# Performance work log

Hardware: AMD Instinct MI355X
Metric: run time of the kernel (lower is better)

Reference implementation:

```python
import jax, jax.numpy as jnp
import numpy as np

N_NODES = 100000
N_EDGES = 250000
EMB = 32
NUM_RELS2 = 100   # 2 * num_rels
NUM_TYPES = 16


def _xavier(key, shape):
    fan_in, fan_out = shape[-2], shape[-1]
    limit = float(np.sqrt(6.0 / (fan_in + fan_out)))
    return jax.random.uniform(key, shape, jnp.float32, -limit, limit)


def setup_inputs() -> dict:
    key = jax.random.key(0)
    ks = jax.random.split(key, 9)
    src_ids = jax.random.randint(ks[0], (N_NODES,), 0, N_NODES)
    edge_src = jax.random.randint(ks[1], (N_EDGES,), 0, N_NODES)
    edge_dst = jax.random.randint(ks[2], (N_EDGES,), 0, N_NODES)
    etype = jax.random.randint(ks[3], (N_EDGES,), 0, NUM_RELS2)
    entity = _xavier(ks[4], (N_NODES, EMB))
    W1 = _xavier(ks[5], (NUM_RELS2, EMB, EMB))
    W2 = _xavier(ks[6], (NUM_RELS2, EMB, NUM_TYPES))
    lambda_w = _xavier(ks[7], (NUM_TYPES, 1))
    lambda_b = jnp.zeros((1,), jnp.float32)
    return {
        "entity": entity, "W1": W1, "W2": W2,
        "lambda_w": lambda_w, "lambda_b": lambda_b,
        "src_ids": src_ids, "edge_src": edge_src,
        "edge_dst": edge_dst, "etype": etype,
    }


def _rgcn_layer(h, W, edge_src, edge_dst, etype, n_dst, activation):
    # gather per-edge relation weights [E, in, out] and per-edge bmm (as DGL does)
    msg = jnp.einsum('ed,edo->eo', h[edge_src], W[etype])  # [E, out]
    s = jax.ops.segment_sum(msg, edge_dst, num_segments=n_dst)  # [N, out]
    deg = jax.ops.segment_sum(jnp.ones((msg.shape[0],), msg.dtype),
                              edge_dst, num_segments=n_dst)
    out = s / jnp.maximum(deg, 1.0)[:, None]  # mean; 0 for isolated dst nodes
    if activation is not None:
        out = activation(out)
    return out


def reference(entity, W1, W2, lambda_w, lambda_b,
              src_ids, edge_src, edge_dst, etype):
    # eval mode: dropout disabled; self_loop=False, bias=False
    h = entity[src_ids]                                            # [N, EMB]
    h = _rgcn_layer(h, W1, edge_src, edge_dst, etype, N_NODES, jax.nn.relu)
    h = _rgcn_layer(h, W2, edge_src, edge_dst, etype, N_NODES, None)  # [N, T]
    # PonderNet loop, max_steps=2: step1 lambda from linear+sigmoid, step2 lambda=1
    lam = jax.nn.sigmoid(h @ lambda_w + lambda_b)[:, 0]            # [N]
    p = jnp.stack([lam, 1.0 - lam])                                # [2, N]
    # recomputed h at step 2 is identical (same params, no dropout)
    y = jnp.stack([h, h])                                          # [2, N, T]
    return (y, p)
```

## Files before the change

kernel.cpp:

```cpp
#include <hip/hip_runtime.h>
#include <hip/hip_bf16.h>

#define N_NODES 100000
#define N_EDGES 250000
#define EMB 32
#define TYPES 16
#define R2 100
#define SB 1024
#define NB ((N_EDGES + SB - 1) / SB)
#define CAP 4096
#define CAPD 16
#define S1 64
#define S2 64
#define LW 4

typedef __attribute__((ext_vector_type(8))) short short8;
typedef __attribute__((ext_vector_type(4))) float f32x4;

__device__ __forceinline__ unsigned short f2bf_u(float f) {
    unsigned u = __float_as_uint(f);
    u = (u + 0x7fffu + ((u >> 16) & 1u)) >> 16;
    return (unsigned short)u;
}
__device__ __forceinline__ float bfl(unsigned u) { return __uint_as_float(u << 16); }
__device__ __forceinline__ float bfh(unsigned u) { return __uint_as_float(u & 0xffff0000u); }

__global__ __launch_bounds__(SB) void pass1_kernel(
        const int* __restrict__ etype, const int* __restrict__ edge_src,
        const int* __restrict__ edge_dst, const int* __restrict__ src_ids,
        const float* __restrict__ W1, const float* __restrict__ W2,
        int* __restrict__ rcnt, int* __restrict__ dcnt,
        unsigned short* __restrict__ pw1, unsigned short* __restrict__ pw2,
        uint2* __restrict__ epack) {
    int t = threadIdx.x, b = blockIdx.x;
    if (b < NB) {
        __shared__ int lh[R2];
        __shared__ int lbase[R2];
        if (t < R2) lh[t] = 0;
        __syncthreads();
        int e = b * SB + t;
        int r = 0, lrank = 0, pd = 0, s = 0, sid = 0;
        bool valid = e < N_EDGES;
        if (valid) {
            r = etype[e];
            lrank = atomicAdd(&lh[r], 1);
            int d = edge_dst[e];
            int drank = atomicAdd(&dcnt[d], 1);
            if (drank > CAPD - 1) drank = CAPD - 1;
            pd = (d << 4) | drank;
            s = edge_src[e];
            sid = src_ids[s];
        }
        __syncthreads();
        if (t < R2) {
            int c = lh[t];
            lbase[t] = c ? atomicAdd(&rcnt[t], c) : 0;
        }
        __syncthreads();
        if (valid) {
            uint2 v = { (unsigned)sid | (((unsigned)pd & 0x7FFFu) << 17),
                        (unsigned)s   | (((unsigned)pd >> 15) << 17) };
            epack[((size_t)r << 12) + lbase[r] + lrank] = v;
        }
    } else {
        int r = b - NB;
        const float* Wr1 = W1 + (size_t)r * (EMB * EMB);
        {
            int l = t >> 4, j = t & 15;
            int n = l & 15, q = l >> 4;
            int k = q * 8 + (j & 7);
            int col = (j < 8) ? (2 * n) : (2 * n + 1);
            pw1[(size_t)r * 1024 + t] = f2bf_u(Wr1[k * EMB + col]);
        }
        if (t < 512) {
            const float* Wr2 = W2 + (size_t)r * (EMB * TYPES);
            int l = t >> 3, j = t & 7;
            int n = l & 15, q = l >> 4;
            int k = q * 8 + j;
            pw2[(size_t)r * 512 + t] = f2bf_u(Wr2[k * TYPES + n]);
        }
    }
}

__global__ __launch_bounds__(64 * LW) void layer1_kernel(
        const float* __restrict__ entity,
        const unsigned short* __restrict__ pw1,
        const int* __restrict__ rcnt,
        const uint2* __restrict__ epack,
        unsigned int* __restrict__ msg1) {
    int r = blockIdx.x % R2, sg = blockIdx.x / R2;
    int lane = threadIdx.x & 63, w = threadIdx.x >> 6;
    int stripe = sg * LW + w;
    int cnt = rcnt[r];
    int nT = (cnt + 15) >> 4;
    int n = lane & 15, q = lane >> 4;
    const unsigned short* pw = pw1 + (size_t)r * 1024;
    short8 b0 = *(const short8*)(pw + lane * 16);
    short8 b1 = *(const short8*)(pw + lane * 16 + 8);
    const uint2* ep = epack + ((size_t)r << 12);
    for (int g = stripe; g < nT; g += S1) {
        int base = g * 16;
        int cl = cnt - base;
        int me = n < cl ? n : cl - 1;
        uint2 E = ep[base + me];
        int sid = (int)(E.x & 0x1FFFFu);
        int pd  = (int)((E.x >> 17) | ((E.y >> 17) << 15));
        const float4* ar = (const float4*)(entity + (size_t)sid * EMB + q * 8);
        float4 v0 = ar[0], v1 = ar[1];
        short8 a;
        a[0] = (short)f2bf_u(v0.x); a[1] = (short)f2bf_u(v0.y);
        a[2] = (short)f2bf_u(v0.z); a[3] = (short)f2bf_u(v0.w);
        a[4] = (short)f2bf_u(v1.x); a[5] = (short)f2bf_u(v1.y);
        a[6] = (short)f2bf_u(v1.z); a[7] = (short)f2bf_u(v1.w);
        f32x4 c0 = {0.f,0.f,0.f,0.f}, c1 = {0.f,0.f,0.f,0.f};
        c0 = __builtin_amdgcn_mfma_f32_16x16x32_bf16(a, b0, c0, 0, 0, 0);
        c1 = __builtin_amdgcn_mfma_f32_16x16x32_bf16(a, b1, c1, 0, 0, 0);
#pragma unroll
        for (int i = 0; i < 4; ++i) {
            int row = q * 4 + i;
            int p = __shfl(pd, row);
            if (row < cl) {
                unsigned wv = (unsigned)f2bf_u(c0[i]) | ((unsigned)f2bf_u(c1[i]) << 16);
                msg1[(size_t)p * 16 + n] = wv;
            }
        }
    }
}

__global__ void reduce1_kernel(const unsigned int* __restrict__ msg1,
                               const int* __restrict__ dcnt,
                               unsigned int* __restrict__ h1bf) {
    int t = blockIdx.x * blockDim.x + threadIdx.x;
    if (t >= N_NODES * 16) return;
    int nn = t >> 4, cp = t & 15;
    int cnt = dcnt[nn];
    int km = cnt < CAPD ? cnt : CAPD;
    int s = nn << 4;
    float sx = 0.f, sy = 0.f;
    for (int k = 0; k < km; ++k) {
        unsigned v = msg1[(size_t)(s + k) * 16 + cp];
        sx += bfl(v); sy += bfh(v);
    }
    float inv = 1.0f / fmaxf((float)cnt, 1.0f);
    unsigned lo = f2bf_u(fmaxf(sx * inv, 0.f));
    unsigned hi = f2bf_u(fmaxf(sy * inv, 0.f));
    h1bf[t] = lo | (hi << 16);
}

__global__ __launch_bounds__(64 * LW) void layer2_kernel(
        const unsigned short* __restrict__ h1bf,
        const unsigned short* __restrict__ pw2,
        const int* __restrict__ rcnt,
        const uint2* __restrict__ epack,
        unsigned int* __restrict__ msg2) {
    int r = blockIdx.x % R2, sg = blockIdx.x / R2;
    int lane = threadIdx.x & 63, w = threadIdx.x >> 6;
    int stripe = sg * LW + w;
    int cnt = rcnt[r];
    int nT = (cnt + 15) >> 4;
    int n = lane & 15, q = lane >> 4;
    short8 b = *(const short8*)(pw2 + (size_t)r * 512 + lane * 8);
    const uint2* ep = epack + ((size_t)r << 12);
    for (int g = stripe; g < nT; g += S2) {
        int base = g * 16;
        int cl = cnt - base;
        int me = n < cl ? n : cl - 1;
        uint2 E = ep[base + me];
        int s  = (int)(E.y & 0x1FFFFu);
        int pd = (int)((E.x >> 17) | ((E.y >> 17) << 15));
        short8 a = *(const short8*)(h1bf + (size_t)s * EMB + q * 8);
        f32x4 c = {0.f,0.f,0.f,0.f};
        c = __builtin_amdgcn_mfma_f32_16x16x32_bf16(a, b, c, 0, 0, 0);
#pragma unroll
        for (int i = 0; i < 4; ++i) {
            int row = q * 4 + i;
            int p = __shfl(pd, row);
            unsigned myb = (unsigned)f2bf_u(c[i]);
            unsigned ob  = (unsigned)__shfl_xor((int)myb, 1);
            if (row < cl && !(n & 1)) {
                msg2[(size_t)p * 8 + (n >> 1)] = myb | (ob << 16);
            }
        }
    }
}

__global__ void reduce2_head_kernel(const unsigned int* __restrict__ msg2,
                                    const int* __restrict__ dcnt,
                                    const float* __restrict__ lw,
                                    const float* __restrict__ lb,
                                    float* __restrict__ out) {
    int nn = blockIdx.x * blockDim.x + threadIdx.x;
    if (nn >= N_NODES) return;
    int cnt = dcnt[nn];
    int km = cnt < CAPD ? cnt : CAPD;
    int s = nn << 4;
    float h[TYPES];
#pragma unroll
    for (int j = 0; j < TYPES; ++j) h[j] = 0.f;
    for (int k = 0; k < km; ++k) {
        const uint4* row = (const uint4*)(msg2 + (size_t)(s + k) * 8);
        uint4 A = row[0], B = row[1];
        h[0] += bfl(A.x);  h[1] += bfh(A.x);  h[2] += bfl(A.y);  h[3] += bfh(A.y);
        h[4] += bfl(A.z);  h[5] += bfh(A.z);  h[6] += bfl(A.w);  h[7] += bfh(A.w);
        h[8] += bfl(B.x);  h[9] += bfh(B.x);  h[10] += bfl(B.y); h[11] += bfh(B.y);
        h[12] += bfl(B.z); h[13] += bfh(B.z); h[14] += bfl(B.w); h[15] += bfh(B.w);
    }
    float inv = 1.0f / fmaxf((float)cnt, 1.0f);
    float dot = 0.f;
#pragma unroll
    for (int j = 0; j < TYPES; ++j) { h[j] *= inv; dot += h[j] * lw[j]; }
    dot += lb[0];
    float lam = 1.0f / (1.0f + expf(-dot));

    float4* y0 = (float4*)(out + (size_t)nn * TYPES);
    float4* y1 = (float4*)(out + (size_t)N_NODES * TYPES + (size_t)nn * TYPES);
#pragma unroll
    for (int j = 0; j < 4; ++j) {
        float4 v = { h[4*j], h[4*j+1], h[4*j+2], h[4*j+3] };
        y0[j] = v; y1[j] = v;
    }
    out[(size_t)2 * N_NODES * TYPES + nn] = lam;
    out[(size_t)2 * N_NODES * TYPES + N_NODES + nn] = 1.0f - lam;
}

extern "C" void kernel_launch(void* const* d_in, const int* in_sizes, int n_in,
                              void* d_out, int out_size, void* d_ws, size_t ws_size,
                              hipStream_t stream) {
    const float* entity = (const float*)d_in[0];
    const float* W1     = (const float*)d_in[1];
    const float* W2     = (const float*)d_in[2];
    const float* lw     = (const float*)d_in[3];
    const float* lb     = (const float*)d_in[4];
    const int* src_ids  = (const int*)d_in[5];
    const int* edge_src = (const int*)d_in[6];
    const int* edge_dst = (const int*)d_in[7];
    const int* etype    = (const int*)d_in[8];
    float* out = (float*)d_out;

    unsigned int* W = (unsigned int*)d_ws;
    int* dcnt   = (int*)(W + 0);
    int* rcnt   = (int*)(W + 100000);
    uint2* epack = (uint2*)(W + 100128);
    unsigned short* pw1 = (unsigned short*)(W + 919328);
    unsigned short* pw2 = (unsigned short*)(W + 970528);
    unsigned int* h1bf  = W + 996128;
    unsigned int* msg1  = W + 2596128;
    unsigned int* msg2  = W + 28196128;

    (void)hipMemsetAsync(d_ws, 0, 100128 * sizeof(int), stream);

    pass1_kernel<<<NB + R2, SB, 0, stream>>>(etype, edge_src, edge_dst, src_ids,
                                             W1, W2, rcnt, dcnt, pw1, pw2, epack);
    layer1_kernel<<<R2 * (S1 / LW), 64 * LW, 0, stream>>>(
        entity, pw1, rcnt, epack, msg1);
    reduce1_kernel<<<(N_NODES * 16 + 255) / 256, 256, 0, stream>>>(msg1, dcnt, h1bf);
    layer2_kernel<<<R2 * (S2 / LW), 64 * LW, 0, stream>>>(
        (const unsigned short*)h1bf, pw2, rcnt, epack, msg2);
    reduce2_head_kernel<<<(N_NODES + 255) / 256, 256, 0, stream>>>(
        msg2, dcnt, lw, lb, out);
}
```

Baseline: 131.7 us.

## Store messages in relation-sorted order and gather via per-destination index table

The per-edge message buffers are now written contiguously in relation-bucket order rather than scattered into dst*16+rank slots. A new eidx table maps each destination slot to its bucket position, and the two reduce kernels gather through it. This turns the scattered writes in the layer kernels into coalesced writes and shrinks the msg buffers. The cost is that the reduce kernels now read scattered rows instead of contiguous ones, plus one extra index read.

```diff
diff --git a/kernel.cpp b/kernel.cpp
--- a/kernel.cpp
+++ b/kernel.cpp
@@ -31,7 +31,8 @@
         const float* __restrict__ W1, const float* __restrict__ W2,
         int* __restrict__ rcnt, int* __restrict__ dcnt,
         unsigned short* __restrict__ pw1, unsigned short* __restrict__ pw2,
-        uint2* __restrict__ epack) {
+        unsigned* __restrict__ esrc1, unsigned* __restrict__ esrc2,
+        unsigned* __restrict__ eidx) {
     int t = threadIdx.x, b = blockIdx.x;
     if (b < NB) {
         __shared__ int lh[R2];
@@ -39,15 +40,14 @@
         if (t < R2) lh[t] = 0;
         __syncthreads();
         int e = b * SB + t;
-        int r = 0, lrank = 0, pd = 0, s = 0, sid = 0;
+        int r = 0, lrank = 0, d = 0, drank = 0, s = 0, sid = 0;
         bool valid = e < N_EDGES;
         if (valid) {
             r = etype[e];
             lrank = atomicAdd(&lh[r], 1);
-            int d = edge_dst[e];
-            int drank = atomicAdd(&dcnt[d], 1);
+            d = edge_dst[e];
+            drank = atomicAdd(&dcnt[d], 1);
             if (drank > CAPD - 1) drank = CAPD - 1;
-            pd = (d << 4) | drank;
             s = edge_src[e];
             sid = src_ids[s];
         }
@@ -58,9 +58,10 @@
         }
         __syncthreads();
         if (valid) {
-            uint2 v = { (unsigned)sid | (((unsigned)pd & 0x7FFFu) << 17),
-                        (unsigned)s   | (((unsigned)pd >> 15) << 17) };
-            epack[((size_t)r << 12) + lbase[r] + lrank] = v;
+            unsigned gp = ((unsigned)r << 12) + (unsigned)(lbase[r] + lrank);
+            esrc1[gp] = (unsigned)sid;
+            esrc2[gp] = (unsigned)s;
+            eidx[(d << 4) | drank] = gp;
         }
     } else {
         int r = b - NB;
@@ -86,7 +87,7 @@
         const float* __restrict__ entity,
         const unsigned short* __restrict__ pw1,
         const int* __restrict__ rcnt,
-        const uint2* __restrict__ epack,
+        const unsigned* __restrict__ esrc1,
         unsigned int* __restrict__ msg1) {
     int r = blockIdx.x % R2, sg = blockIdx.x / R2;
     int lane = threadIdx.x & 63, w = threadIdx.x >> 6;
@@ -97,14 +98,12 @@
     const unsigned short* pw = pw1 + (size_t)r * 1024;
     short8 b0 = *(const short8*)(pw + lane * 16);
     short8 b1 = *(const short8*)(pw + lane * 16 + 8);
-    const uint2* ep = epack + ((size_t)r << 12);
+    const unsigned* es = esrc1 + ((size_t)r << 12);
     for (int g = stripe; g < nT; g += S1) {
         int base = g * 16;
         int cl = cnt - base;
         int me = n < cl ? n : cl - 1;
-        uint2 E = ep[base + me];
-        int sid = (int)(E.x & 0x1FFFFu);
-        int pd  = (int)((E.x >> 17) | ((E.y >> 17) << 15));
+        int sid = (int)es[base + me];
         const float4* ar = (const float4*)(entity + (size_t)sid * EMB + q * 8);
         float4 v0 = ar[0], v1 = ar[1];
         short8 a;
@@ -115,19 +114,20 @@
         f32x4 c0 = {0.f,0.f,0.f,0.f}, c1 = {0.f,0.f,0.f,0.f};
         c0 = __builtin_amdgcn_mfma_f32_16x16x32_bf16(a, b0, c0, 0, 0, 0);
         c1 = __builtin_amdgcn_mfma_f32_16x16x32_bf16(a, b1, c1, 0, 0, 0);
+        size_t rowbase = ((size_t)(r << 12) + base) * 16;
 #pragma unroll
         for (int i = 0; i < 4; ++i) {
             int row = q * 4 + i;
-            int p = __shfl(pd, row);
             if (row < cl) {
                 unsigned wv = (unsigned)f2bf_u(c0[i]) | ((unsigned)f2bf_u(c1[i]) << 16);
-                msg1[(size_t)p * 16 + n] = wv;
+                msg1[rowbase + (size_t)row * 16 + n] = wv;
             }
         }
     }
 }
 
 __global__ void reduce1_kernel(const unsigned int* __restrict__ msg1,
+                               const unsigned* __restrict__ eidx,
                                const int* __restrict__ dcnt,
                                unsigned int* __restrict__ h1bf) {
     int t = blockIdx.x * blockDim.x + threadIdx.x;
@@ -135,10 +135,11 @@
     int nn = t >> 4, cp = t & 15;
     int cnt = dcnt[nn];
     int km = cnt < CAPD ? cnt : CAPD;
-    int s = nn << 4;
+    int myidx = (int)eidx[t];
     float sx = 0.f, sy = 0.f;
     for (int k = 0; k < km; ++k) {
-        unsigned v = msg1[(size_t)(s + k) * 16 + cp];
+        int idx = __shfl(myidx, k, 16);
+        unsigned v = msg1[(size_t)idx * 16 + cp];
         sx += bfl(v); sy += bfh(v);
     }
     float inv = 1.0f / fmaxf((float)cnt, 1.0f);
@@ -151,7 +152,7 @@
         const unsigned short* __restrict__ h1bf,
         const unsigned short* __restrict__ pw2,
         const int* __restrict__ rcnt,
-        const uint2* __restrict__ epack,
+        const unsigned* __restrict__ esrc2,
         unsigned int* __restrict__ msg2) {
     int r = blockIdx.x % R2, sg = blockIdx.x / R2;
     int lane = threadIdx.x & 63, w = threadIdx.x >> 6;
@@ -160,31 +161,30 @@
     int nT = (cnt + 15) >> 4;
     int n = lane & 15, q = lane >> 4;
     short8 b = *(const short8*)(pw2 + (size_t)r * 512 + lane * 8);
-    const uint2* ep = epack + ((size_t)r << 12);
+    const unsigned* es = esrc2 + ((size_t)r << 12);
     for (int g = stripe; g < nT; g += S2) {
         int base = g * 16;
         int cl = cnt - base;
         int me = n < cl ? n : cl - 1;
-        uint2 E = ep[base + me];
-        int s  = (int)(E.y & 0x1FFFFu);
-        int pd = (int)((E.x >> 17) | ((E.y >> 17) << 15));
+        int s = (int)es[base + me];
         short8 a = *(const short8*)(h1bf + (size_t)s * EMB + q * 8);
         f32x4 c = {0.f,0.f,0.f,0.f};
         c = __builtin_amdgcn_mfma_f32_16x16x32_bf16(a, b, c, 0, 0, 0);
+        size_t rowbase = ((size_t)(r << 12) + base) * 8;
 #pragma unroll
         for (int i = 0; i < 4; ++i) {
             int row = q * 4 + i;
-            int p = __shfl(pd, row);
             unsigned myb = (unsigned)f2bf_u(c[i]);
             unsigned ob  = (unsigned)__shfl_xor((int)myb, 1);
             if (row < cl && !(n & 1)) {
-                msg2[(size_t)p * 8 + (n >> 1)] = myb | (ob << 16);
+                msg2[rowbase + (size_t)row * 8 + (n >> 1)] = myb | (ob << 16);
             }
         }
     }
 }
 
 __global__ void reduce2_head_kernel(const unsigned int* __restrict__ msg2,
+                                    const unsigned* __restrict__ eidx,
                                     const int* __restrict__ dcnt,
                                     const float* __restrict__ lw,
                                     const float* __restrict__ lb,
@@ -193,12 +193,17 @@
     if (nn >= N_NODES) return;
     int cnt = dcnt[nn];
     int km = cnt < CAPD ? cnt : CAPD;
-    int s = nn << 4;
+    const uint4* ei = (const uint4*)(eidx + ((size_t)nn << 4));
+    uint4 I0 = ei[0], I1 = ei[1], I2 = ei[2], I3 = ei[3];
+    unsigned idxs[16] = { I0.x, I0.y, I0.z, I0.w, I1.x, I1.y, I1.z, I1.w,
+                          I2.x, I2.y, I2.z, I2.w, I3.x, I3.y, I3.z, I3.w };
     float h[TYPES];
 #pragma unroll
     for (int j = 0; j < TYPES; ++j) h[j] = 0.f;
-    for (int k = 0; k < km; ++k) {
-        const uint4* row = (const uint4*)(msg2 + (size_t)(s + k) * 8);
+#pragma unroll
+    for (int k = 0; k < 16; ++k) {
+        if (k >= km) break;
+        const uint4* row = (const uint4*)(msg2 + (size_t)idxs[k] * 8);
         uint4 A = row[0], B = row[1];
         h[0] += bfl(A.x);  h[1] += bfh(A.x);  h[2] += bfl(A.y);  h[3] += bfh(A.y);
         h[4] += bfl(A.z);  h[5] += bfh(A.z);  h[6] += bfl(A.w);  h[7] += bfh(A.w);
@@ -238,24 +243,28 @@
     float* out = (float*)d_out;
 
     unsigned int* W = (unsigned int*)d_ws;
-    int* dcnt   = (int*)(W + 0);
-    int* rcnt   = (int*)(W + 100000);
-    uint2* epack = (uint2*)(W + 100128);
-    unsigned short* pw1 = (unsigned short*)(W + 919328);
-    unsigned short* pw2 = (unsigned short*)(W + 970528);
-    unsigned int* h1bf  = W + 996128;
-    unsigned int* msg1  = W + 2596128;
-    unsigned int* msg2  = W + 28196128;
+    int* dcnt        = (int*)(W + 0);
+    int* rcnt        = (int*)(W + 100000);
+    unsigned* esrc1  = W + 100128;
+    unsigned* esrc2  = W + 509728;
+    unsigned* eidx   = W + 919328;
+    unsigned short* pw1 = (unsigned short*)(W + 2519328);
+    unsigned short* pw2 = (unsigned short*)(W + 2570528);
+    unsigned int* h1bf  = W + 2596128;
+    unsigned int* msg1  = W + 4196128;
+    unsigned int* msg2  = W + 10749728;
 
     (void)hipMemsetAsync(d_ws, 0, 100128 * sizeof(int), stream);
 
     pass1_kernel<<<NB + R2, SB, 0, stream>>>(etype, edge_src, edge_dst, src_ids,
-                                             W1, W2, rcnt, dcnt, pw1, pw2, epack);
+                                             W1, W2, rcnt, dcnt, pw1, pw2,
+                                             esrc1, esrc2, eidx);
     layer1_kernel<<<R2 * (S1 / LW), 64 * LW, 0, stream>>>(
-        entity, pw1, rcnt, epack, msg1);
-    reduce1_kernel<<<(N_NODES * 16 + 255) / 256, 256, 0, stream>>>(msg1, dcnt, h1bf);
+        entity, pw1, rcnt, esrc1, msg1);
+    reduce1_kernel<<<(N_NODES * 16 + 255) / 256, 256, 0, stream>>>(
+        msg1, eidx, dcnt, h1bf);
     layer2_kernel<<<R2 * (S2 / LW), 64 * LW, 0, stream>>>(
-        (const unsigned short*)h1bf, pw2, rcnt, epack, msg2);
+        (const unsigned short*)h1bf, pw2, rcnt, esrc2, msg2);
     reduce2_head_kernel<<<(N_NODES + 255) / 256, 256, 0, stream>>>(
-        msg2, dcnt, lw, lb, out);
-}
+        msg2, eidx, dcnt, lw, lb, out);
+}
```

Result: slower. 137.1 us (+4.1%).

## Unroll reduce loops with clamped loads and widen layer grid stripes

Applied to the files above, without the earlier changes.

The per-node reduction loops in both reduce kernels are unrolled (by 4 and by 2), with indices clamped and masks applied, so several independent gathers are in flight at once instead of a serial dependent chain. The S1/S2 stripe constants are also raised from 64 to 192, which changes how the layer kernels split each relation's edges across blocks. The clamped loads may re-read the same row, and the different grid split could change occupancy and load balance.

```diff
diff --git a/kernel.cpp b/kernel.cpp
--- a/kernel.cpp
+++ b/kernel.cpp
@@ -10,8 +10,8 @@
 #define NB ((N_EDGES + SB - 1) / SB)
 #define CAP 4096
 #define CAPD 16
-#define S1 64
-#define S2 64
+#define S1 192
+#define S2 192
 #define LW 4
 
 typedef __attribute__((ext_vector_type(8))) short short8;
@@ -137,9 +137,21 @@
     int km = cnt < CAPD ? cnt : CAPD;
     int s = nn << 4;
     float sx = 0.f, sy = 0.f;
-    for (int k = 0; k < km; ++k) {
-        unsigned v = msg1[(size_t)(s + k) * 16 + cp];
-        sx += bfl(v); sy += bfh(v);
+    for (int k0 = 0; k0 < km; k0 += 4) {
+        int kmax = km - 1;
+        int i0 = k0,     c0 = i0 < kmax ? i0 : kmax;
+        int i1 = k0 + 1, c1 = i1 < kmax ? i1 : kmax;
+        int i2 = k0 + 2, c2 = i2 < kmax ? i2 : kmax;
+        int i3 = k0 + 3, c3 = i3 < kmax ? i3 : kmax;
+        unsigned v0 = msg1[(size_t)(s + c0) * 16 + cp];
+        unsigned v1 = msg1[(size_t)(s + c1) * 16 + cp];
+        unsigned v2 = msg1[(size_t)(s + c2) * 16 + cp];
+        unsigned v3 = msg1[(size_t)(s + c3) * 16 + cp];
+        float m1 = (i1 < km) ? 1.f : 0.f;
+        float m2 = (i2 < km) ? 1.f : 0.f;
+        float m3 = (i3 < km) ? 1.f : 0.f;
+        sx += bfl(v0) + m1 * bfl(v1) + m2 * bfl(v2) + m3 * bfl(v3);
+        sy += bfh(v0) + m1 * bfh(v1) + m2 * bfh(v2) + m3 * bfh(v3);
     }
     float inv = 1.0f / fmaxf((float)cnt, 1.0f);
     unsigned lo = f2bf_u(fmaxf(sx * inv, 0.f));
@@ -197,13 +209,20 @@
     float h[TYPES];
 #pragma unroll
     for (int j = 0; j < TYPES; ++j) h[j] = 0.f;
-    for (int k = 0; k < km; ++k) {
-        const uint4* row = (const uint4*)(msg2 + (size_t)(s + k) * 8);
-        uint4 A = row[0], B = row[1];
-        h[0] += bfl(A.x);  h[1] += bfh(A.x);  h[2] += bfl(A.y);  h[3] += bfh(A.y);
-        h[4] += bfl(A.z);  h[5] += bfh(A.z);  h[6] += bfl(A.w);  h[7] += bfh(A.w);
-        h[8] += bfl(B.x);  h[9] += bfh(B.x);  h[10] += bfl(B.y); h[11] += bfh(B.y);
-        h[12] += bfl(B.z); h[13] += bfh(B.z); h[14] += bfl(B.w); h[15] += bfh(B.w);
+    for (int k = 0; k < km; k += 2) {
+        int k1 = (k + 1 < km) ? k + 1 : k;
+        float m1 = (k + 1 < km) ? 1.f : 0.f;
+        const uint4* r0 = (const uint4*)(msg2 + (size_t)(s + k) * 8);
+        const uint4* r1 = (const uint4*)(msg2 + (size_t)(s + k1) * 8);
+        uint4 A0 = r0[0], B0 = r0[1], A1 = r1[0], B1 = r1[1];
+        h[0] += bfl(A0.x) + m1 * bfl(A1.x);  h[1] += bfh(A0.x) + m1 * bfh(A1.x);
+        h[2] += bfl(A0.y) + m1 * bfl(A1.y);  h[3] += bfh(A0.y) + m1 * bfh(A1.y);
+        h[4] += bfl(A0.z) + m1 * bfl(A1.z);  h[5] += bfh(A0.z) + m1 * bfh(A1.z);
+        h[6] += bfl(A0.w) + m1 * bfl(A1.w);  h[7] += bfh(A0.w) + m1 * bfh(A1.w);
+        h[8] += bfl(B0.x) + m1 * bfl(B1.x);  h[9] += bfh(B0.x) + m1 * bfh(B1.x);
+        h[10] += bfl(B0.y) + m1 * bfl(B1.y); h[11] += bfh(B0.y) + m1 * bfh(B1.y);
+        h[12] += bfl(B0.z) + m1 * bfl(B1.z); h[13] += bfh(B0.z) + m1 * bfh(B1.z);
+        h[14] += bfl(B0.w) + m1 * bfl(B1.w); h[15] += bfh(B0.w) + m1 * bfh(B1.w);
     }
     float inv = 1.0f / fmaxf((float)cnt, 1.0f);
     float dot = 0.f;
```

Measured after the change: 129.0 us. -2.1%, faster.
